# Performance work log

Measured on AMD Instinct MI355X. Metric: run time of the kernel, lower is better.

The kernel has to match this reference:

```python
import jax, jax.numpy as jnp
import numpy as np

N_EMBED = 8192
EMBED_DIM = 128
BETA = 1.0
DECAY = 0.99
EPS = 1e-5


def l2norm(t, eps=1e-12):
    # matches F.normalize(p=2, dim=-1)
    n = jnp.linalg.norm(t, axis=-1, keepdims=True)
    return t / jnp.maximum(n, eps)


def setup_inputs() -> dict:
    key = jax.random.key(0)
    k1, k2 = jax.random.split(key)
    z = jax.random.normal(k1, (16, 1024, EMBED_DIM), dtype=jnp.float32)
    embedding = l2norm(jax.random.normal(k2, (N_EMBED, EMBED_DIM), dtype=jnp.float32))
    cluster_size = jnp.zeros((N_EMBED,), dtype=jnp.float32)
    embed_avg = embedding.copy()
    return {"z": z, "embedding": embedding, "cluster_size": cluster_size, "embed_avg": embed_avg}


def reference(z, embedding, cluster_size, embed_avg):
    z_input = z
    zn = l2norm(z)
    zf = zn.reshape(-1, EMBED_DIM)  # [N, d]

    # pairwise squared L2 distances to codebook: [N, n_embed]
    d = (jnp.sum(zf * zf, axis=1, keepdims=True)
         + jnp.sum(embedding * embedding, axis=1)
         - 2.0 * jnp.einsum('bd,nd->bn', zf, embedding))
    encoding_indices = jnp.argmin(d, axis=1)  # [N]

    z_q = embedding[encoding_indices].reshape(zn.shape)
    loss = BETA * jnp.mean((jax.lax.stop_gradient(z_q) - zn) ** 2)

    # EMA update (training branch) -- one-hot scatter expressed as segment sums
    bins = jax.ops.segment_sum(jnp.ones_like(encoding_indices, dtype=zf.dtype),
                               encoding_indices, num_segments=N_EMBED)  # [n_embed]
    new_cluster_size = cluster_size * DECAY + (1.0 - DECAY) * bins

    embed_sum = jax.ops.segment_sum(zf, encoding_indices, num_segments=N_EMBED)  # [n_embed, d]
    embed_normalized = l2norm(embed_sum / (bins[:, None] + EPS))
    embed_normalized = jnp.where((bins == 0)[:, None], embedding, embed_normalized)
    new_embed_avg = embed_avg * DECAY + (1.0 - DECAY) * embed_normalized
    new_embedding = l2norm(new_embed_avg)

    # straight-through estimator
    z_q = z_input + jax.lax.stop_gradient(z_q - z_input)
    return z_q, loss, encoding_indices, new_embedding, new_cluster_size, new_embed_avg
```

## Files before the change

### kernel.cpp

```cpp
#include <hip/hip_runtime.h>
#include <hip/hip_bf16.h>

constexpr int NV = 16384;
constexpr int D  = 128;
constexpr int NE = 8192;
constexpr float DECAY = 0.99f;
constexpr float BETA  = 1.0f;
constexpr float EPS   = 1e-5f;
constexpr float LO_SCALE     = 4096.0f;
constexpr float INV_LO_SCALE = 1.0f / 4096.0f;

constexpr float QSCALE = 65536.0f;
constexpr float QOFF   = 98304.0f;

constexpr int Q = 4;
constexpr int CODES_PER_Q = NE / Q;
constexpr int SUBT = 32;
constexpr int TILES = CODES_PER_Q / SUBT;
constexpr int BZ = 128;
constexpr int NCAND = Q * 2;

constexpr size_t WS_Z2    = 0;
constexpr size_t WS_E2    = WS_Z2 + (size_t)NV * 128;
constexpr size_t WS_EN2   = WS_E2 + (size_t)NE * 128;
constexpr size_t WS_MINI2 = WS_EN2 + NE;
constexpr size_t WS_BINS  = WS_Z2;
constexpr size_t WS_ESUM  = WS_BINS + NE;
constexpr size_t WS_LPART = WS_ESUM + (size_t)NE * D;

constexpr size_t OUT_ZQ   = 0;
constexpr size_t OUT_LOSS = OUT_ZQ + (size_t)NV*D;
constexpr size_t OUT_IDX  = OUT_LOSS + 1;
constexpr size_t OUT_EMB  = OUT_IDX + NV;
constexpr size_t OUT_CS   = OUT_EMB + (size_t)NE*D;
constexpr size_t OUT_EAVG = OUT_CS + NE;

using half8  = __attribute__((ext_vector_type(8))) _Float16;
using half2v = __attribute__((ext_vector_type(2))) _Float16;
using f32x16 = __attribute__((ext_vector_type(16))) float;

__device__ inline float waveReduceSum(float v) {
    #pragma unroll
    for (int o = 32; o > 0; o >>= 1) v += __shfl_xor(v, o, 64);
    return v;
}
__device__ inline unsigned umin32(unsigned a, unsigned b) { return a < b ? a : b; }
__device__ inline unsigned umax32(unsigned a, unsigned b) { return a > b ? a : b; }

__device__ inline void gload_lds16(const void* g, void* s) {
    __builtin_amdgcn_global_load_lds(
        (const __attribute__((address_space(1))) unsigned int*)g,
        (__attribute__((address_space(3))) unsigned int*)s, 16, 0, 0);
}

__global__ void k_prep(const float* __restrict__ z, const float* __restrict__ emb,
                       _Float16* __restrict__ z2, _Float16* __restrict__ e2h,
                       float* __restrict__ en2) {
    int tid = threadIdx.x;
    int l = tid & 63;
    int g = blockIdx.x * 4 + (tid >> 6);
    bool isZ = g < NV;
    int row = isZ ? g : g - NV;
    const float* src = isZ ? &z[(size_t)row * D] : &emb[(size_t)row * D];

    const float2 v = *reinterpret_cast<const float2*>(&src[l * 2]);
    float s = waveReduceSum(v.x * v.x + v.y * v.y);
    float x0 = v.x, x1 = v.y;
    if (isZ) {
        float inv = 1.0f / fmaxf(sqrtf(s), 1e-12f);
        x0 *= inv; x1 *= inv;
        _Float16 h0 = (_Float16)x0, h1 = (_Float16)x1;
        _Float16 l0 = (_Float16)((x0 - (float)h0) * LO_SCALE);
        _Float16 l1 = (_Float16)((x1 - (float)h1) * LO_SCALE);
        _Float16* zr = &z2[(size_t)row * 256];
        half2v hh = {h0, h1}, lv = {l0, l1};
        *reinterpret_cast<half2v*>(&zr[l * 2])       = hh;
        *reinterpret_cast<half2v*>(&zr[128 + l * 2]) = lv;
    } else {
        if (l == 0) en2[row] = s;
        _Float16 h0 = (_Float16)x0, h1 = (_Float16)x1;
        half2v hh = {h0, h1};
        *reinterpret_cast<half2v*>(&e2h[(size_t)row * 128 + l * 2]) = hh;
    }
}

__global__ __launch_bounds__(256, 2) void k_dist(
        const _Float16* __restrict__ z2, const _Float16* __restrict__ e2h,
        const float* __restrict__ en2, unsigned* __restrict__ minI2) {
    __shared__ _Float16 eb[4][2][SUBT * 128];
    __shared__ float c0s[CODES_PER_Q];

    const int tid = threadIdx.x;
    const int w  = tid >> 6;
    const int l  = tid & 63;
    const int cc = l & 31;
    const int gg = l >> 5;
    const int zb = blockIdx.x * BZ;
    const int q  = blockIdx.y;
    const int cbase0 = q * CODES_PER_Q;

    half8 a_h[8], a_l[8];
    {
        const size_t row = (size_t)(zb + w * 32 + cc);
        #pragma unroll
        for (int kf = 0; kf < 8; ++kf) {
            a_h[kf] = *reinterpret_cast<const half8*>(&z2[row * 256 + kf * 16 + gg * 8]);
            a_l[kf] = *reinterpret_cast<const half8*>(&z2[row * 256 + 128 + kf * 16 + gg * 8]);
        }
    }

    for (int i = tid; i < CODES_PER_Q; i += 256)
        c0s[i] = fmaf(en2[cbase0 + i], QSCALE, QOFF);
    __syncthreads();

    int soff[8];
    #pragma unroll
    for (int i = 0; i < 8; ++i) {
        int c = i * 64 + l;
        int code = c >> 4, slot = c & 15;
        soff[i] = code * 256 + ((slot ^ (code & 7)) * 16);
    }
    auto stage = [&](int b, int t) {
        const char* tbase = reinterpret_cast<const char*>(&e2h[(size_t)(cbase0 + t * SUBT) * 128]);
        #pragma unroll
        for (int i = 0; i < 8; ++i)
            gload_lds16(tbase + soff[i], &eb[w][b][(size_t)i * 512]);
    };

    stage(0, 0);

    unsigned bU1[16], bU2[16];
    #pragma unroll
    for (int i = 0; i < 16; ++i) { bU1[i] = 0xFFFFFFFFu; bU2[i] = 0xFFFFFFFFu; }

    const int swz = cc & 7;

    int cur = 0;
    for (int t = 0; t < TILES; ++t) {
        if (t + 1 < TILES) {
            stage(cur ^ 1, t + 1);
            asm volatile("s_waitcnt vmcnt(8)" ::: "memory");
        } else {
            asm volatile("s_waitcnt vmcnt(0)" ::: "memory");
        }
        __builtin_amdgcn_sched_barrier(0);

        const char* rbase = reinterpret_cast<const char*>(&eb[w][cur][0]) + cc * 256;
        half8 b0 = *reinterpret_cast<const half8*>(rbase + (((0 * 2 + gg) ^ swz) * 16));
        half8 b1 = *reinterpret_cast<const half8*>(rbase + (((1 * 2 + gg) ^ swz) * 16));
        half8 b2 = *reinterpret_cast<const half8*>(rbase + (((2 * 2 + gg) ^ swz) * 16));
        half8 b3 = *reinterpret_cast<const half8*>(rbase + (((3 * 2 + gg) ^ swz) * 16));
        half8 b4 = *reinterpret_cast<const half8*>(rbase + (((4 * 2 + gg) ^ swz) * 16));
        half8 b5 = *reinterpret_cast<const half8*>(rbase + (((5 * 2 + gg) ^ swz) * 16));
        half8 b6 = *reinterpret_cast<const half8*>(rbase + (((6 * 2 + gg) ^ swz) * 16));
        half8 b7 = *reinterpret_cast<const half8*>(rbase + (((7 * 2 + gg) ^ swz) * 16));

        f32x16 accA1{}, accA2{}, accB1{}, accB2{};
        accA1 = __builtin_amdgcn_mfma_f32_32x32x16_f16(a_h[0], b0, accA1, 0, 0, 0);
        accB1 = __builtin_amdgcn_mfma_f32_32x32x16_f16(a_l[0], b0, accB1, 0, 0, 0);
        accA2 = __builtin_amdgcn_mfma_f32_32x32x16_f16(a_h[4], b4, accA2, 0, 0, 0);
        accB2 = __builtin_amdgcn_mfma_f32_32x32x16_f16(a_l[4], b4, accB2, 0, 0, 0);
        accA1 = __builtin_amdgcn_mfma_f32_32x32x16_f16(a_h[1], b1, accA1, 0, 0, 0);
        accB1 = __builtin_amdgcn_mfma_f32_32x32x16_f16(a_l[1], b1, accB1, 0, 0, 0);
        accA2 = __builtin_amdgcn_mfma_f32_32x32x16_f16(a_h[5], b5, accA2, 0, 0, 0);
        accB2 = __builtin_amdgcn_mfma_f32_32x32x16_f16(a_l[5], b5, accB2, 0, 0, 0);
        accA1 = __builtin_amdgcn_mfma_f32_32x32x16_f16(a_h[2], b2, accA1, 0, 0, 0);
        accB1 = __builtin_amdgcn_mfma_f32_32x32x16_f16(a_l[2], b2, accB1, 0, 0, 0);
        accA2 = __builtin_amdgcn_mfma_f32_32x32x16_f16(a_h[6], b6, accA2, 0, 0, 0);
        accB2 = __builtin_amdgcn_mfma_f32_32x32x16_f16(a_l[6], b6, accB2, 0, 0, 0);
        accA1 = __builtin_amdgcn_mfma_f32_32x32x16_f16(a_h[3], b3, accA1, 0, 0, 0);
        accB1 = __builtin_amdgcn_mfma_f32_32x32x16_f16(a_l[3], b3, accB1, 0, 0, 0);
        accA2 = __builtin_amdgcn_mfma_f32_32x32x16_f16(a_h[7], b7, accA2, 0, 0, 0);
        accB2 = __builtin_amdgcn_mfma_f32_32x32x16_f16(a_l[7], b7, accB2, 0, 0, 0);

        const unsigned code = (unsigned)(cbase0 + t * SUBT + cc);
        const float c0 = c0s[t * SUBT + cc];
        #pragma unroll
        for (int r = 0; r < 16; ++r) {
            float sumA = accA1[r] + accA2[r];
            float sumB = accB1[r] + accB2[r];
            float tq = fmaf(-2.0f * QSCALE, sumA, c0);
            tq = fmaf(-2.0f * QSCALE * INV_LO_SCALE, sumB, tq);
            unsigned u = ((unsigned)tq << 13) | code;
            unsigned m1 = bU1[r];
            bU2[r] = umin32(umax32(u, m1), bU2[r]);
            bU1[r] = umin32(u, m1);
        }
        cur ^= 1;
    }

    #pragma unroll
    for (int r = 0; r < 16; ++r) {
        unsigned u1 = bU1[r], u2 = bU2[r];
        #pragma unroll
        for (int m = 1; m < 32; m <<= 1) {
            unsigned o1 = (unsigned)__shfl_xor((int)u1, m, 64);
            unsigned o2 = (unsigned)__shfl_xor((int)u2, m, 64);
            unsigned hi = umax32(u1, o1);
            u1 = umin32(u1, o1);
            u2 = umin32(umin32(u2, o2), hi);
        }
        if (cc == 0) {
            int zrow = zb + w * 32 + (r & 3) + 8 * (r >> 2) + 4 * gg;
            size_t o = ((size_t)zrow * Q + q) * 2;
            minI2[o] = u1; minI2[o + 1] = u2;
        }
    }
}

__global__ void k_gather(const float* __restrict__ z, const float* __restrict__ emb,
                         const float* __restrict__ en2, const unsigned* __restrict__ minI2,
                         float* __restrict__ outZq, float* __restrict__ outIdx,
                         float* __restrict__ bins, float* __restrict__ esum,
                         float* __restrict__ lossPart) {
    __shared__ float zsh[4][128];
    __shared__ float ecs[4][NCAND][132];
    int tid = threadIdx.x;
    int wave = tid >> 6, lane = tid & 63;
    int zr = blockIdx.x * 4 + wave;

    const float2 zv = *reinterpret_cast<const float2*>(&z[(size_t)zr * D + lane * 2]);
    float s = waveReduceSum(zv.x * zv.x + zv.y * zv.y);
    float inv = 1.0f / fmaxf(sqrtf(s), 1e-12f);
    float znx = zv.x * inv, zny = zv.y * inv;
    zsh[wave][lane * 2]     = znx;
    zsh[wave][lane * 2 + 1] = zny;

    int ci = 0x7fffffff;
    if (lane < NCAND) ci = (int)(minI2[(size_t)zr * NCAND + lane] & 8191u);
    #pragma unroll
    for (int c = 0; c < NCAND; ++c) {
        int cc_ = __shfl(ci, c, 64);
        const float2 ev = *reinterpret_cast<const float2*>(&emb[(size_t)cc_ * D + lane * 2]);
        ecs[wave][c][lane * 2]     = ev.x;
        ecs[wave][c][lane * 2 + 1] = ev.y;
    }

    float cv = 3.4e38f;
    if (lane < NCAND) {
        float dot = 0.0f;
        #pragma unroll 8
        for (int k = 0; k < 128; ++k) dot = fmaf(zsh[wave][k], ecs[wave][lane][k], dot);
        cv = fmaf(-2.0f, dot, en2[ci]);
    }
    float bv = cv; int bi = ci;
    #pragma unroll
    for (int m = 1; m < NCAND; m <<= 1) {
        float ov = __shfl_xor(bv, m, 64);
        int   oi = __shfl_xor(bi, m, 64);
        if (ov < bv || (ov == bv && oi < bi)) { bv = ov; bi = oi; }
    }
    bi = __shfl(bi, 0, 64);
    if (lane == 0) outIdx[zr] = (float)bi;

    float2 e = *reinterpret_cast<const float2*>(&emb[(size_t)bi * D + lane * 2]);
    *reinterpret_cast<float2*>(&outZq[(size_t)zr * D + lane * 2]) = e;

    float dx = e.x - znx, dy = e.y - zny;
    float ls = waveReduceSum(dx * dx + dy * dy);

    if (lane == 0) atomicAdd(&bins[bi], 1.0f);
    atomicAdd(&esum[(size_t)bi * D + lane * 2 + 0], znx);
    atomicAdd(&esum[(size_t)bi * D + lane * 2 + 1], zny);

    __shared__ float part[4];
    if (lane == 0) part[wave] = ls;
    __syncthreads();
    if (tid == 0) lossPart[blockIdx.x] = (part[0] + part[1]) + (part[2] + part[3]);
}

__global__ void k_codebook(const float* __restrict__ emb, const float* __restrict__ csz,
                           const float* __restrict__ eavg, const float* __restrict__ bins,
                           const float* __restrict__ esum, const float* __restrict__ lossPart,
                           float* __restrict__ outEmb, float* __restrict__ outCs,
                           float* __restrict__ outEavg, float* __restrict__ outLoss) {
    int tid = threadIdx.x;
    int wave = tid >> 6, lane = tid & 63;
    int n = blockIdx.x * 4 + wave;

    if (blockIdx.x == 0) {
        float s = 0.0f;
        for (int i = tid; i < 4096; i += 256) s += lossPart[i];
        s = waveReduceSum(s);
        __shared__ float p[4];
        if ((tid & 63) == 0) p[tid >> 6] = s;
        __syncthreads();
        if (tid == 0) outLoss[0] = BETA * ((p[0] + p[1]) + (p[2] + p[3])) / (float)((size_t)NV * D);
    }

    float b = bins[n];
    if (lane == 0) outCs[n] = csz[n] * DECAY + (1.0f - DECAY) * b;

    float2 es = *reinterpret_cast<const float2*>(&esum[(size_t)n * D + lane * 2]);
    float invb = 1.0f / (b + EPS);
    float mx = es.x * invb, my = es.y * invb;
    float ss = waveReduceSum(mx * mx + my * my);
    float invn = 1.0f / fmaxf(sqrtf(ss), 1e-12f);

    float2 er = *reinterpret_cast<const float2*>(&emb[(size_t)n * D + lane * 2]);
    float enx = (b == 0.0f) ? er.x : mx * invn;
    float eny = (b == 0.0f) ? er.y : my * invn;

    float2 ea = *reinterpret_cast<const float2*>(&eavg[(size_t)n * D + lane * 2]);
    float nax = ea.x * DECAY + (1.0f - DECAY) * enx;
    float nay = ea.y * DECAY + (1.0f - DECAY) * eny;
    float2 no; no.x = nax; no.y = nay;
    *reinterpret_cast<float2*>(&outEavg[(size_t)n * D + lane * 2]) = no;

    float ss2 = waveReduceSum(nax * nax + nay * nay);
    float inv2 = 1.0f / fmaxf(sqrtf(ss2), 1e-12f);
    float2 ne; ne.x = nax * inv2; ne.y = nay * inv2;
    *reinterpret_cast<float2*>(&outEmb[(size_t)n * D + lane * 2]) = ne;
}

extern "C" void kernel_launch(void* const* d_in, const int* in_sizes, int n_in,
                              void* d_out, int out_size, void* d_ws, size_t ws_size,
                              hipStream_t stream) {
    (void)in_sizes; (void)n_in; (void)out_size; (void)ws_size;
    const float* z    = (const float*)d_in[0];
    const float* emb  = (const float*)d_in[1];
    const float* csz  = (const float*)d_in[2];
    const float* eavg = (const float*)d_in[3];
    float* out = (float*)d_out;
    float* ws  = (float*)d_ws;

    _Float16* z2   = (_Float16*)(ws + WS_Z2);
    _Float16* e2h  = (_Float16*)(ws + WS_E2);
    float*    en2  = ws + WS_EN2;
    unsigned* minI2 = (unsigned*)(ws + WS_MINI2);
    float*  bins   = ws + WS_BINS;
    float*  esum   = ws + WS_ESUM;
    float*  lpart  = ws + WS_LPART;

    k_prep<<<(NV + NE) / 4, 256, 0, stream>>>(z, emb, z2, e2h, en2);
    k_dist<<<dim3(NV / BZ, Q), 256, 0, stream>>>(z2, e2h, en2, minI2);
    hipMemsetAsync(bins, 0, ((size_t)NE + (size_t)NE * D) * sizeof(float), stream);
    k_gather<<<NV / 4, 256, 0, stream>>>(z, emb, en2, minI2,
                                         out + OUT_ZQ, out + OUT_IDX, bins, esum, lpart);
    k_codebook<<<NE / 4, 256, 0, stream>>>(emb, csz, eavg, bins, esum, lpart,
                                           out + OUT_EMB, out + OUT_CS, out + OUT_EAVG,
                                           out + OUT_LOSS);
}
```

Measured before the change: 142.6 us.

## Replace direct global-to-LDS double buffering with register-prefetched single LDS buffer

The codebook tile staging in the distance kernel no longer uses async global_load_lds into two LDS buffers. Each tile is now prefetched into registers (eight float4 per lane) during compute and written to a single per-wave LDS buffer after the distance/argmin step. This halves LDS use and drops the explicit vmcnt waits, at the cost of extra VGPRs and LDS writes through registers. The four split MFMA accumulators are also merged into two, which frees registers but makes each accumulator chain twice as long and more serial.

Result: slower. 286.9 us (+101.1%).

```diff
diff --git a/kernel.cpp b/kernel.cpp
--- a/kernel.cpp
+++ b/kernel.cpp
@@ -46,12 +46,6 @@
 }
 __device__ inline unsigned umin32(unsigned a, unsigned b) { return a < b ? a : b; }
 __device__ inline unsigned umax32(unsigned a, unsigned b) { return a > b ? a : b; }
-
-__device__ inline void gload_lds16(const void* g, void* s) {
-    __builtin_amdgcn_global_load_lds(
-        (const __attribute__((address_space(1))) unsigned int*)g,
-        (__attribute__((address_space(3))) unsigned int*)s, 16, 0, 0);
-}
 
 __global__ void k_prep(const float* __restrict__ z, const float* __restrict__ emb,
                        _Float16* __restrict__ z2, _Float16* __restrict__ e2h,
@@ -87,7 +81,7 @@
 __global__ __launch_bounds__(256, 2) void k_dist(
         const _Float16* __restrict__ z2, const _Float16* __restrict__ e2h,
         const float* __restrict__ en2, unsigned* __restrict__ minI2) {
-    __shared__ _Float16 eb[4][2][SUBT * 128];
+    __shared__ _Float16 eb[4][SUBT * 128];
     __shared__ float c0s[CODES_PER_Q];
 
     const int tid = threadIdx.x;
@@ -120,14 +114,21 @@
         int code = c >> 4, slot = c & 15;
         soff[i] = code * 256 + ((slot ^ (code & 7)) * 16);
     }
-    auto stage = [&](int b, int t) {
-        const char* tbase = reinterpret_cast<const char*>(&e2h[(size_t)(cbase0 + t * SUBT) * 128]);
+    _Float16* ebw = eb[w];
+    auto tbase = [&](int t) {
+        return reinterpret_cast<const char*>(&e2h[(size_t)(cbase0 + t * SUBT) * 128]);
+    };
+
+    float4 p[8];
+    {
+        const char* tb = tbase(0);
         #pragma unroll
         for (int i = 0; i < 8; ++i)
-            gload_lds16(tbase + soff[i], &eb[w][b][(size_t)i * 512]);
-    };
-
-    stage(0, 0);
+            p[i] = *reinterpret_cast<const float4*>(tb + soff[i]);
+        #pragma unroll
+        for (int i = 0; i < 8; ++i)
+            *reinterpret_cast<float4*>(reinterpret_cast<char*>(ebw) + i * 1024 + l * 16) = p[i];
+    }
 
     unsigned bU1[16], bU2[16];
     #pragma unroll
@@ -135,17 +136,15 @@
 
     const int swz = cc & 7;
 
-    int cur = 0;
     for (int t = 0; t < TILES; ++t) {
         if (t + 1 < TILES) {
-            stage(cur ^ 1, t + 1);
-            asm volatile("s_waitcnt vmcnt(8)" ::: "memory");
-        } else {
-            asm volatile("s_waitcnt vmcnt(0)" ::: "memory");
-        }
-        __builtin_amdgcn_sched_barrier(0);
-
-        const char* rbase = reinterpret_cast<const char*>(&eb[w][cur][0]) + cc * 256;
+            const char* tb = tbase(t + 1);
+            #pragma unroll
+            for (int i = 0; i < 8; ++i)
+                p[i] = *reinterpret_cast<const float4*>(tb + soff[i]);
+        }
+
+        const char* rbase = reinterpret_cast<const char*>(ebw) + cc * 256;
         half8 b0 = *reinterpret_cast<const half8*>(rbase + (((0 * 2 + gg) ^ swz) * 16));
         half8 b1 = *reinterpret_cast<const half8*>(rbase + (((1 * 2 + gg) ^ swz) * 16));
         half8 b2 = *reinterpret_cast<const half8*>(rbase + (((2 * 2 + gg) ^ swz) * 16));
@@ -155,38 +154,41 @@
         half8 b6 = *reinterpret_cast<const half8*>(rbase + (((6 * 2 + gg) ^ swz) * 16));
         half8 b7 = *reinterpret_cast<const half8*>(rbase + (((7 * 2 + gg) ^ swz) * 16));
 
-        f32x16 accA1{}, accA2{}, accB1{}, accB2{};
-        accA1 = __builtin_amdgcn_mfma_f32_32x32x16_f16(a_h[0], b0, accA1, 0, 0, 0);
-        accB1 = __builtin_amdgcn_mfma_f32_32x32x16_f16(a_l[0], b0, accB1, 0, 0, 0);
-        accA2 = __builtin_amdgcn_mfma_f32_32x32x16_f16(a_h[4], b4, accA2, 0, 0, 0);
-        accB2 = __builtin_amdgcn_mfma_f32_32x32x16_f16(a_l[4], b4, accB2, 0, 0, 0);
-        accA1 = __builtin_amdgcn_mfma_f32_32x32x16_f16(a_h[1], b1, accA1, 0, 0, 0);
-        accB1 = __builtin_amdgcn_mfma_f32_32x32x16_f16(a_l[1], b1, accB1, 0, 0, 0);
-        accA2 = __builtin_amdgcn_mfma_f32_32x32x16_f16(a_h[5], b5, accA2, 0, 0, 0);
-        accB2 = __builtin_amdgcn_mfma_f32_32x32x16_f16(a_l[5], b5, accB2, 0, 0, 0);
-        accA1 = __builtin_amdgcn_mfma_f32_32x32x16_f16(a_h[2], b2, accA1, 0, 0, 0);
-        accB1 = __builtin_amdgcn_mfma_f32_32x32x16_f16(a_l[2], b2, accB1, 0, 0, 0);
-        accA2 = __builtin_amdgcn_mfma_f32_32x32x16_f16(a_h[6], b6, accA2, 0, 0, 0);
-        accB2 = __builtin_amdgcn_mfma_f32_32x32x16_f16(a_l[6], b6, accB2, 0, 0, 0);
-        accA1 = __builtin_amdgcn_mfma_f32_32x32x16_f16(a_h[3], b3, accA1, 0, 0, 0);
-        accB1 = __builtin_amdgcn_mfma_f32_32x32x16_f16(a_l[3], b3, accB1, 0, 0, 0);
-        accA2 = __builtin_amdgcn_mfma_f32_32x32x16_f16(a_h[7], b7, accA2, 0, 0, 0);
-        accB2 = __builtin_amdgcn_mfma_f32_32x32x16_f16(a_l[7], b7, accB2, 0, 0, 0);
+        f32x16 accA{}, accB{};
+        accA = __builtin_amdgcn_mfma_f32_32x32x16_f16(a_h[0], b0, accA, 0, 0, 0);
+        accB = __builtin_amdgcn_mfma_f32_32x32x16_f16(a_l[0], b0, accB, 0, 0, 0);
+        accA = __builtin_amdgcn_mfma_f32_32x32x16_f16(a_h[1], b1, accA, 0, 0, 0);
+        accB = __builtin_amdgcn_mfma_f32_32x32x16_f16(a_l[1], b1, accB, 0, 0, 0);
+        accA = __builtin_amdgcn_mfma_f32_32x32x16_f16(a_h[2], b2, accA, 0, 0, 0);
+        accB = __builtin_amdgcn_mfma_f32_32x32x16_f16(a_l[2], b2, accB, 0, 0, 0);
+        accA = __builtin_amdgcn_mfma_f32_32x32x16_f16(a_h[3], b3, accA, 0, 0, 0);
+        accB = __builtin_amdgcn_mfma_f32_32x32x16_f16(a_l[3], b3, accB, 0, 0, 0);
+        accA = __builtin_amdgcn_mfma_f32_32x32x16_f16(a_h[4], b4, accA, 0, 0, 0);
+        accB = __builtin_amdgcn_mfma_f32_32x32x16_f16(a_l[4], b4, accB, 0, 0, 0);
+        accA = __builtin_amdgcn_mfma_f32_32x32x16_f16(a_h[5], b5, accA, 0, 0, 0);
+        accB = __builtin_amdgcn_mfma_f32_32x32x16_f16(a_l[5], b5, accB, 0, 0, 0);
+        accA = __builtin_amdgcn_mfma_f32_32x32x16_f16(a_h[6], b6, accA, 0, 0, 0);
+        accB = __builtin_amdgcn_mfma_f32_32x32x16_f16(a_l[6], b6, accB, 0, 0, 0);
+        accA = __builtin_amdgcn_mfma_f32_32x32x16_f16(a_h[7], b7, accA, 0, 0, 0);
+        accB = __builtin_amdgcn_mfma_f32_32x32x16_f16(a_l[7], b7, accB, 0, 0, 0);
 
         const unsigned code = (unsigned)(cbase0 + t * SUBT + cc);
         const float c0 = c0s[t * SUBT + cc];
         #pragma unroll
         for (int r = 0; r < 16; ++r) {
-            float sumA = accA1[r] + accA2[r];
-            float sumB = accB1[r] + accB2[r];
-            float tq = fmaf(-2.0f * QSCALE, sumA, c0);
-            tq = fmaf(-2.0f * QSCALE * INV_LO_SCALE, sumB, tq);
+            float tq = fmaf(-2.0f * QSCALE, accA[r],
+                            fmaf(-2.0f * QSCALE * INV_LO_SCALE, accB[r], c0));
             unsigned u = ((unsigned)tq << 13) | code;
             unsigned m1 = bU1[r];
             bU2[r] = umin32(umax32(u, m1), bU2[r]);
             bU1[r] = umin32(u, m1);
         }
-        cur ^= 1;
+
+        if (t + 1 < TILES) {
+            #pragma unroll
+            for (int i = 0; i < 8; ++i)
+                *reinterpret_cast<float4*>(reinterpret_cast<char*>(ebw) + i * 1024 + l * 16) = p[i];
+        }
     }
 
     #pragma unroll
```
